# Kernel optimization log

Hardware: AMD Instinct MI355X
Metric: run time of the kernel (lower is better)

## Reference

```python
import jax, jax.numpy as jnp
import numpy as np

B, S, D, H = 2, 2048, 512, 8
HD = D // H  # head_size = 64
EPS = 1e-5


def _layer_norm(x, g, b):
    m = jnp.mean(x, axis=-1, keepdims=True)
    v = jnp.mean(jnp.square(x - m), axis=-1, keepdims=True)
    return (x - m) * jax.lax.rsqrt(v + EPS) * g + b


def setup_inputs() -> dict:
    key = jax.random.key(0)
    ks = jax.random.split(key, 16)
    s_in = 1.0 / np.sqrt(D)
    s_ff = 1.0 / np.sqrt(4 * D)
    return {
        "x": jax.random.normal(ks[0], (B, S, D), jnp.float32),
        # per-head q/k/v projections stacked over heads: [H, D, HD]
        "Wq": jax.random.normal(ks[1], (H, D, HD), jnp.float32) * s_in,
        "bq": jax.random.normal(ks[2], (H, HD), jnp.float32) * s_in,
        "Wk": jax.random.normal(ks[3], (H, D, HD), jnp.float32) * s_in,
        "bk": jax.random.normal(ks[4], (H, HD), jnp.float32) * s_in,
        "Wv": jax.random.normal(ks[5], (H, D, HD), jnp.float32) * s_in,
        "bv": jax.random.normal(ks[6], (H, HD), jnp.float32) * s_in,
        "Wp": jax.random.normal(ks[7], (D, D), jnp.float32) * s_in,
        "bp": jax.random.normal(ks[8], (D,), jnp.float32) * s_in,
        "W1": jax.random.normal(ks[9], (D, 4 * D), jnp.float32) * s_in,
        "b1": jax.random.normal(ks[10], (4 * D,), jnp.float32) * s_in,
        "W2": jax.random.normal(ks[11], (4 * D, D), jnp.float32) * s_ff,
        "b2": jax.random.normal(ks[12], (D,), jnp.float32) * s_ff,
        "g1": jnp.ones((D,), jnp.float32),
        "be1": jnp.zeros((D,), jnp.float32),
        "g2": jnp.ones((D,), jnp.float32),
        "be2": jnp.zeros((D,), jnp.float32),
    }


def reference(x, Wq, bq, Wk, bk, Wv, bv, Wp, bp, W1, b1, W2, b2, g1, be1, g2, be2):
    # --- attention sublayer (pre-norm) ---
    xn = _layer_norm(x, g1, be1)                               # [B,S,D]
    q = jnp.einsum('bsd,hde->bhse', xn, Wq) + bq[None, :, None, :]
    k = jnp.einsum('bsd,hde->bhse', xn, Wk) + bk[None, :, None, :]
    v = jnp.einsum('bsd,hde->bhse', xn, Wv) + bv[None, :, None, :]
    # NOTE: original has NO 1/sqrt(head_size) scaling and NO mask
    scores = jnp.einsum('bhse,bhte->bhst', q, k)               # [B,H,S,S]
    w = jax.nn.softmax(scores, axis=-1)
    o = jnp.einsum('bhst,bhte->bhse', w, v)                    # [B,H,S,HD]
    o = o.transpose(0, 2, 1, 3).reshape(x.shape[0], x.shape[1], D)  # concat heads
    attn_out = o @ Wp + bp
    x = x + attn_out
    # --- MLP sublayer (pre-norm) ---
    xn2 = _layer_norm(x, g2, be2)
    h = jax.nn.relu(xn2 @ W1 + b1)
    x = x + (h @ W2 + b2)
    return x
```

## Files before the change

kernel.cpp:

```cpp
#include <hip/hip_runtime.h>
#include <hip/hip_bf16.h>

typedef unsigned short u16;
typedef unsigned long long u64t;
typedef __attribute__((ext_vector_type(8))) short bhalf8;
typedef __attribute__((ext_vector_type(4))) short bhalf4;
typedef __attribute__((ext_vector_type(4))) float f32x4;

#define MFMA16(a, b, c) __builtin_amdgcn_mfma_f32_16x16x32_bf16((a), (b), (c), 0, 0, 0)

#if __has_builtin(__builtin_amdgcn_mfma_f32_16x16x16bf16_1k)
#define HAVE_K16 1
#define MFMAK16(a, b, c) __builtin_amdgcn_mfma_f32_16x16x16bf16_1k((a), (b), (c), 0, 0, 0)
#elif __has_builtin(__builtin_amdgcn_mfma_f32_16x16x16_bf16)
#define HAVE_K16 1
#define MFMAK16(a, b, c) __builtin_amdgcn_mfma_f32_16x16x16_bf16((a), (b), (c), 0, 0, 0)
#else
#define HAVE_K16 0
#endif

#if __has_builtin(__builtin_amdgcn_perm)
#define HAVE_PERM 1
#else
#define HAVE_PERM 0
#endif

#define BB 2
#define SS 2048
#define DD 512
#define HH 8
#define HD 64
#define NT (BB * SS)
#define LOG2E 1.44269504f

#if __has_builtin(__builtin_amdgcn_exp2f)
#define EXP2(x) __builtin_amdgcn_exp2f(x)
#else
#define EXP2(x) exp2f(x)
#endif

__device__ __forceinline__ u16 f2b(float f) {
    unsigned u = __builtin_bit_cast(unsigned, f);
    unsigned r = (u + 0x7fffu + ((u >> 16) & 1u)) >> 16;
    return (u16)r;
}

__device__ __forceinline__ unsigned pk2bf(float f0, float f1) {
#if HAVE_PERM
    unsigned a0 = __builtin_bit_cast(unsigned, f0) + 0x8000u;
    unsigned a1 = __builtin_bit_cast(unsigned, f1) + 0x8000u;
    return __builtin_amdgcn_perm(a1, a0, 0x07060302u);
#else
    return (unsigned)f2b(f0) | ((unsigned)f2b(f1) << 16);
#endif
}

__device__ __forceinline__ void gl2lds16(const u16* g, u16* l) {
    u16* gn = (u16*)g;
    __builtin_amdgcn_global_load_lds((__attribute__((address_space(1))) void*)gn,
                                     (__attribute__((address_space(3))) void*)l, 16, 0, 0);
}

__global__ __launch_bounds__(256) void k_prep(const float* __restrict__ Wq, const float* __restrict__ Wk,
                                              const float* __restrict__ Wv, const float* __restrict__ Wp,
                                              const float* __restrict__ W1, const float* __restrict__ W2,
                                              const float* __restrict__ bq, const float* __restrict__ bk,
                                              const float* __restrict__ bv,
                                              u16* __restrict__ WqkvT, u16* __restrict__ WpT,
                                              u16* __restrict__ W1T, u16* __restrict__ W2T,
                                              float* __restrict__ biasqkv,
                                              const float* __restrict__ x, const float* __restrict__ g1,
                                              const float* __restrict__ be1, u16* __restrict__ xn) {
    int j = blockIdx.x;
    int t = threadIdx.x;
    if (j >= 3078) {
        int wave = t >> 6, lane = t & 63;
        int row = (j - 3078) * 4 + wave;
        const float* xr = x + (size_t)row * DD;
        int c = lane * 8;
        float4 v0 = *(const float4*)(xr + c);
        float4 v1 = *(const float4*)(xr + c + 4);
        float s  = v0.x + v0.y + v0.z + v0.w + v1.x + v1.y + v1.z + v1.w;
        float sq = v0.x*v0.x + v0.y*v0.y + v0.z*v0.z + v0.w*v0.w
                 + v1.x*v1.x + v1.y*v1.y + v1.z*v1.z + v1.w*v1.w;
#pragma unroll
        for (int m = 1; m < 64; m <<= 1) {
            s  += __shfl_xor(s, m);
            sq += __shfl_xor(sq, m);
        }
        float mean = s * (1.0f / DD);
        float var  = sq * (1.0f / DD) - mean * mean;
        float rstd = rsqrtf(var + 1e-5f);
        float4 g0 = *(const float4*)(g1 + c);
        float4 g4 = *(const float4*)(g1 + c + 4);
        float4 b0 = *(const float4*)(be1 + c);
        float4 b4 = *(const float4*)(be1 + c + 4);
        float xv[8] = {v0.x, v0.y, v0.z, v0.w, v1.x, v1.y, v1.z, v1.w};
        float gv[8] = {g0.x, g0.y, g0.z, g0.w, g4.x, g4.y, g4.z, g4.w};
        float bv2[8] = {b0.x, b0.y, b0.z, b0.w, b4.x, b4.y, b4.z, b4.w};
        union { bhalf8 v; u16 u[8]; } pk;
#pragma unroll
        for (int i = 0; i < 8; i++) pk.u[i] = f2b((xv[i] - mean) * rstd * gv[i] + bv2[i]);
        *(bhalf8*)(xn + (size_t)row * DD + c) = pk.v;
        return;
    }
    int tx = t & 31, ty = t >> 5;
    if (j >= 3072) {
        int i = (j - 3072) * 256 + ty * 32 + tx;
        biasqkv[i] = (i < 512) ? bq[i] : (i < 1024) ? bk[i - 512] : bv[i - 1024];
        return;
    }
    __shared__ float tile[32][33];
    const float* src; u16* dst; int R, C, tr, tc;
    if (j < 768) {
        int m = j >> 8, rem = j & 255, h = rem >> 5, tl = rem & 31;
        tr = tl >> 1; tc = tl & 1;
        src = (m == 0 ? Wq : (m == 1 ? Wk : Wv)) + h * 32768;
        dst = WqkvT + m * 262144 + h * 32768;
        R = 512; C = 64;
    } else if (j < 1024) { int tl = j - 768;  tr = tl >> 4; tc = tl & 15; src = Wp; dst = WpT; R = 512;  C = 512;  }
    else if (j < 2048)   { int tl = j - 1024; tr = tl >> 6; tc = tl & 63; src = W1; dst = W1T; R = 512;  C = 2048; }
    else                 { int tl = j - 2048; tr = tl >> 4; tc = tl & 15; src = W2; dst = W2T; R = 2048; C = 512;  }
    int c = tc * 32 + tx;
#pragma unroll
    for (int i = 0; i < 4; i++)
        tile[ty + i * 8][tx] = src[(size_t)(tr * 32 + ty + i * 8) * C + c];
    __syncthreads();
    int r2 = tr * 32 + tx;
#pragma unroll
    for (int i = 0; i < 4; i++)
        dst[(size_t)(tc * 32 + ty + i * 8) * R + r2] = f2b(tile[tx][ty + i * 8]);
}

__global__ __launch_bounds__(256) void k_layernorm(const float* __restrict__ x,
                                                   const float* __restrict__ g,
                                                   const float* __restrict__ be,
                                                   u16* __restrict__ out) {
    int wave = threadIdx.x >> 6, lane = threadIdx.x & 63;
    int row = blockIdx.x * 4 + wave;
    const float* xr = x + (size_t)row * DD;
    int c = lane * 8;
    float4 v0 = *(const float4*)(xr + c);
    float4 v1 = *(const float4*)(xr + c + 4);
    float s  = v0.x + v0.y + v0.z + v0.w + v1.x + v1.y + v1.z + v1.w;
    float sq = v0.x*v0.x + v0.y*v0.y + v0.z*v0.z + v0.w*v0.w
             + v1.x*v1.x + v1.y*v1.y + v1.z*v1.z + v1.w*v1.w;
#pragma unroll
    for (int m = 1; m < 64; m <<= 1) {
        s  += __shfl_xor(s, m);
        sq += __shfl_xor(sq, m);
    }
    float mean = s * (1.0f / DD);
    float var  = sq * (1.0f / DD) - mean * mean;
    float rstd = rsqrtf(var + 1e-5f);
    float4 g0 = *(const float4*)(g + c);
    float4 g1 = *(const float4*)(g + c + 4);
    float4 b0 = *(const float4*)(be + c);
    float4 b1 = *(const float4*)(be + c + 4);
    float xv[8] = {v0.x, v0.y, v0.z, v0.w, v1.x, v1.y, v1.z, v1.w};
    float gv[8] = {g0.x, g0.y, g0.z, g0.w, g1.x, g1.y, g1.z, g1.w};
    float bv[8] = {b0.x, b0.y, b0.z, b0.w, b1.x, b1.y, b1.z, b1.w};
    union { bhalf8 v; u16 u[8]; } pk;
#pragma unroll
    for (int i = 0; i < 8; i++) pk.u[i] = f2b((xv[i] - mean) * rstd * gv[i] + bv[i]);
    *(bhalf8*)(out + (size_t)row * DD + c) = pk.v;
}

template<int BM, int BN, int WR, int WC, int MI, int NI, int MODE>
__global__ __launch_bounds__(256) void k_gemm(const u16* __restrict__ A, const u16* __restrict__ Bt,
                                              const float* __restrict__ bias,
                                              int lda, int ldb, int kLen, int N,
                                              const float* __restrict__ resid,
                                              float* __restrict__ outF, u16* __restrict__ outB,
                                              u16* __restrict__ qd, u16* __restrict__ kd,
                                              u16* __restrict__ vtd) {
    constexpr int WM = MI * 16;
    constexpr int WN = NI * 16;
    static_assert(WR * WM == BM && WC * WN == BN && WR * WC == 4, "cfg");
    constexpr int ACH = BM / 32;
    constexpr int BCH = BN / 32;
    __shared__ u16 As0[BM * 64];
    __shared__ u16 Bs0[BN * 64];
    __shared__ u16 As1[BM * 64];
    __shared__ u16 Bs1[BN * 64];
    int t = threadIdx.x;
    int wave = t >> 6, lane = t & 63, quad = lane >> 4, l16 = lane & 15;
    int wr, wc;
    if (WC == 1)      { wr = wave; wc = 0; }
    else if (WR == 1) { wr = 0;    wc = wave; }
    else              { wr = wave >> 1; wc = wave & 1; }
    int m0 = blockIdx.y * BM, n0 = blockIdx.x * BN;

    f32x4 acc[MI][NI] = {};

    int srow = lane >> 3;
    int scol = (lane & 7) * 8;
    const u16* Ag = A  + (size_t)(m0 + srow) * lda + scol;
    const u16* Bg = Bt + (size_t)(n0 + srow) * ldb + scol;

    auto stage = [&](u16* Asd, u16* Bsd, int k0) {
#pragma unroll
        for (int c = 0; c < ACH; c++) {
            int ch = wave * ACH + c;
            gl2lds16(Ag + (size_t)(ch * 8) * lda + k0, &Asd[ch * 512]);
        }
#pragma unroll
        for (int c = 0; c < BCH; c++) {
            int ch = wave * BCH + c;
            gl2lds16(Bg + (size_t)(ch * 8) * ldb + k0, &Bsd[ch * 512]);
        }
    };
    auto compute = [&](const u16* Asd, const u16* Bsd) {
#pragma unroll
        for (int h = 0; h < 2; h++) {
            bhalf8 af[MI], bf[NI];
#pragma unroll
            for (int mi = 0; mi < MI; mi++)
                af[mi] = *(const bhalf8*)&Asd[(wr * WM + mi * 16 + l16) * 64 + h * 32 + quad * 8];
#pragma unroll
            for (int ni = 0; ni < NI; ni++)
                bf[ni] = *(const bhalf8*)&Bsd[(wc * WN + ni * 16 + l16) * 64 + h * 32 + quad * 8];
#pragma unroll
            for (int mi = 0; mi < MI; mi++)
#pragma unroll
                for (int ni = 0; ni < NI; ni++)
                    acc[mi][ni] = MFMA16(af[mi], bf[ni], acc[mi][ni]);
        }
    };

    int nt = kLen >> 6;
    stage(As0, Bs0, 0);
    __syncthreads();
    for (int kt = 0; kt < nt; kt += 2) {
        if (kt + 1 < nt) stage(As1, Bs1, (kt + 1) << 6);
        compute(As0, Bs0);
        __syncthreads();
        if (kt + 1 < nt) {
            if (kt + 2 < nt) stage(As0, Bs0, (kt + 2) << 6);
            compute(As1, Bs1);
            __syncthreads();
        }
    }

#pragma unroll
    for (int mi = 0; mi < MI; mi++)
#pragma unroll
        for (int ni = 0; ni < NI; ni++) {
            f32x4 a = acc[mi][ni];
            int gc = n0 + wc * WN + ni * 16 + l16;
            int gr0 = m0 + wr * WM + mi * 16 + quad * 4;
            float bsv = bias[gc];
            if (MODE == 0) {
                int mm = gc >> 9, cc = gc & 511;
                int hh = cc >> 6, e = cc & 63;
                int b = gr0 >> 11, s0 = gr0 & 2047;
                if (mm == 2) {
                    u64t pk = 0;
#pragma unroll
                    for (int r = 0; r < 4; r++) pk |= (u64t)f2b(a[r] + bsv) << (16 * r);
                    *(u64t*)&vtd[((size_t)(b * HH + hh) * HD + e) * SS + s0] = pk;
                } else if (mm == 0) {
#pragma unroll
                    for (int r = 0; r < 4; r++)
                        qd[((size_t)(b * HH + hh) * SS + s0 + r) * HD + e] = f2b((a[r] + bsv) * LOG2E);
                } else {
#pragma unroll
                    for (int r = 0; r < 4; r++)
                        kd[((size_t)(b * HH + hh) * SS + s0 + r) * HD + e] = f2b(a[r] + bsv);
                }
            } else if (MODE == 1) {
#pragma unroll
                for (int r = 0; r < 4; r++) {
                    size_t idx = (size_t)(gr0 + r) * N + gc;
                    outF[idx] = a[r] + bsv + resid[idx];
                }
            } else {
#pragma unroll
                for (int r = 0; r < 4; r++)
                    outB[(size_t)(gr0 + r) * N + gc] = f2b(fmaxf(a[r] + bsv, 0.0f));
            }
        }
}

__global__ __launch_bounds__(512) void k_attention(const u16* __restrict__ q,
                                                   const u16* __restrict__ k,
                                                   const u16* __restrict__ vt,
                                                   float* __restrict__ Opart,
                                                   float* __restrict__ lsum) {
    __shared__ u16 sm[35840];
    u16* Ks0 = sm;
    u16* Vs0 = sm + 9216;
    u16* Ks1 = sm + 17920;
    u16* Vs1 = sm + 27136;
    float* Ored = (float*)sm;
    float* Lred = (float*)sm + 8192;

    int bh = blockIdx.x, qt = blockIdx.y, kspl = blockIdx.z;
    int t = threadIdx.x, wave = t >> 6, lane = t & 63, quad = lane >> 4, l16 = lane & 15;
    int g = wave >> 2, qw = wave & 3;
    const u16* qb = q  + (size_t)bh * SS * HD;
    const u16* kb = k  + (size_t)bh * SS * HD;
    const u16* vb = vt + (size_t)bh * HD * SS;

    bhalf8 qfa0, qfa1, qfb0, qfb1;
    {
        int r0 = qt * 128 + qw * 32 + l16;
        qfa0 = *(const bhalf8*)(qb + (size_t)r0 * HD + quad * 8);
        qfa1 = *(const bhalf8*)(qb + (size_t)r0 * HD + 32 + quad * 8);
        qfb0 = *(const bhalf8*)(qb + (size_t)(r0 + 16) * HD + quad * 8);
        qfb1 = *(const bhalf8*)(qb + (size_t)(r0 + 16) * HD + 32 + quad * 8);
    }

    f32x4 oacc[2][4] = {};
    f32x4 rsa4 = {}, rsb4 = {};

    int kr = t >> 2, kc = (t & 3) * 16;
    int vr = t >> 3, vc = (t & 7) * 16;
    const u16* kp = kb + ((size_t)kspl * 1024 + kr) * HD + kc;
    const u16* vp = vb + (size_t)vr * SS + kspl * 1024 + vc;
    int koff = kr * 72 + kc;
    int voff = vr * 136 + vc;

    bhalf8 kreg[2], vreg[2];
#pragma unroll
    for (int i = 0; i < 2; i++) {
        kreg[i] = *(const bhalf8*)(kp + i * 8);
        vreg[i] = *(const bhalf8*)(vp + i * 8);
    }
#pragma unroll
    for (int i = 0; i < 2; i++) {
        *(bhalf8*)(&Ks0[koff] + i * 8) = kreg[i];
        *(bhalf8*)(&Vs0[voff] + i * 8) = vreg[i];
    }
    __syncthreads();
#pragma unroll
    for (int i = 0; i < 2; i++) {
        kreg[i] = *(const bhalf8*)(kp + (size_t)128 * HD + i * 8);
        vreg[i] = *(const bhalf8*)(vp + 128 + i * 8);
    }

    auto att_step = [&](const u16* Ksb, const u16* Vsb) {
#pragma unroll
        for (int nt2 = 0; nt2 < 4; nt2++) {
            int nt = g * 4 + nt2;
            bhalf8 kf0 = *(const bhalf8*)&Ksb[(nt * 16 + l16) * 72 + quad * 8];
            bhalf8 kf1 = *(const bhalf8*)&Ksb[(nt * 16 + l16) * 72 + 32 + quad * 8];
            f32x4 sa = {}, sb = {};
            __builtin_amdgcn_s_setprio(1);
            sa = MFMA16(kf0, qfa0, sa);
            sa = MFMA16(kf1, qfa1, sa);
            sb = MFMA16(kf0, qfb0, sb);
            sb = MFMA16(kf1, qfb1, sb);
            __builtin_amdgcn_s_setprio(0);
#if HAVE_K16
            float p0[4], p1[4];
#pragma unroll
            for (int r = 0; r < 4; r++) {
                p0[r] = EXP2(sa[r]);
                p1[r] = EXP2(sb[r]);
            }
#pragma unroll
            for (int r = 0; r < 4; r++) { rsa4[r] += p0[r]; rsb4[r] += p1[r]; }
            union { bhalf4 v; unsigned w[2]; } pa, pb;
            pa.w[0] = pk2bf(p0[0], p0[1]);
            pa.w[1] = pk2bf(p0[2], p0[3]);
            pb.w[0] = pk2bf(p1[0], p1[1]);
            pb.w[1] = pk2bf(p1[2], p1[3]);
            __builtin_amdgcn_s_setprio(1);
#pragma unroll
            for (int et = 0; et < 4; et++) {
                bhalf4 vf = *(const bhalf4*)&Vsb[(et * 16 + l16) * 136 + nt * 16 + quad * 4];
                oacc[0][et] = MFMAK16(pa.v, vf, oacc[0][et]);
                oacc[1][et] = MFMAK16(pb.v, vf, oacc[1][et]);
            }
            __builtin_amdgcn_s_setprio(0);
#else
            float p0[4], p1[4];
#pragma unroll
            for (int r = 0; r < 4; r++) {
                p0[r] = EXP2(sa[r]);
                p1[r] = EXP2(sb[r]);
                rsa4[r] += p0[r]; rsb4[r] += p1[r];
            }
            union { bhalf8 v; unsigned w[4]; } pa, pb;
            pa.w[0] = pk2bf(p0[0], p0[1]);
            pa.w[1] = pk2bf(p0[2], p0[3]);
            pa.w[2] = 0; pa.w[3] = 0;
            pb.w[0] = pk2bf(p1[0], p1[1]);
            pb.w[1] = pk2bf(p1[2], p1[3]);
            pb.w[2] = 0; pb.w[3] = 0;
            __builtin_amdgcn_s_setprio(1);
#pragma unroll
            for (int et = 0; et < 4; et++) {
                union { bhalf8 v; bhalf4 h[2]; } vf;
                vf.h[0] = *(const bhalf4*)&Vsb[(et * 16 + l16) * 136 + nt * 16 + quad * 4];
                vf.h[1] = (bhalf4){0, 0, 0, 0};
                oacc[0][et] = MFMA16(pa.v, vf.v, oacc[0][et]);
                oacc[1][et] = MFMA16(pb.v, vf.v, oacc[1][et]);
            }
            __builtin_amdgcn_s_setprio(0);
#endif
        }
    };

    for (int it = 0; it < 8; it += 2) {
#pragma unroll
        for (int i = 0; i < 2; i++) {
            *(bhalf8*)(&Ks1[koff] + i * 8) = kreg[i];
            *(bhalf8*)(&Vs1[voff] + i * 8) = vreg[i];
        }
        if (it + 2 < 8) {
            const u16* kn = kp + (size_t)(it + 2) * 128 * HD;
            const u16* vn = vp + (it + 2) * 128;
#pragma unroll
            for (int i = 0; i < 2; i++) {
                kreg[i] = *(const bhalf8*)(kn + i * 8);
                vreg[i] = *(const bhalf8*)(vn + i * 8);
            }
        }
        att_step(Ks0, Vs0);
        __syncthreads();
        if (it + 2 < 8) {
#pragma unroll
            for (int i = 0; i < 2; i++) {
                *(bhalf8*)(&Ks0[koff] + i * 8) = kreg[i];
                *(bhalf8*)(&Vs0[voff] + i * 8) = vreg[i];
            }
            if (it + 3 < 8) {
                const u16* kn = kp + (size_t)(it + 3) * 128 * HD;
                const u16* vn = vp + (it + 3) * 128;
#pragma unroll
                for (int i = 0; i < 2; i++) {
                    kreg[i] = *(const bhalf8*)(kn + i * 8);
                    vreg[i] = *(const bhalf8*)(vn + i * 8);
                }
            }
        }
        att_step(Ks1, Vs1);
        __syncthreads();
    }

    float rsa = (rsa4[0] + rsa4[1]) + (rsa4[2] + rsa4[3]);
    float rsb = (rsb4[0] + rsb4[1]) + (rsb4[2] + rsb4[3]);
    rsa += __shfl_xor(rsa, 16); rsa += __shfl_xor(rsa, 32);
    rsb += __shfl_xor(rsb, 16); rsb += __shfl_xor(rsb, 32);

    if (g == 1) {
#pragma unroll
        for (int qc = 0; qc < 2; qc++)
#pragma unroll
            for (int et = 0; et < 4; et++)
#pragma unroll
                for (int r = 0; r < 4; r++)
                    Ored[(qw * 32 + qc * 16 + quad * 4 + r) * 64 + et * 16 + l16] = oacc[qc][et][r];
        if (quad == 0) {
            Lred[qw * 32 + l16]      = rsa;
            Lred[qw * 32 + 16 + l16] = rsb;
        }
    }
    __syncthreads();
    if (g == 0) {
#pragma unroll
        for (int qc = 0; qc < 2; qc++) {
            int sbase = qt * 128 + qw * 32 + qc * 16;
            float* Ob = Opart + ((size_t)(kspl * 16 + bh) * SS + sbase) * HD;
#pragma unroll
            for (int et = 0; et < 4; et++)
#pragma unroll
                for (int r = 0; r < 4; r++) {
                    float v = oacc[qc][et][r]
                            + Ored[(qw * 32 + qc * 16 + quad * 4 + r) * 64 + et * 16 + l16];
                    Ob[(quad * 4 + r) * HD + et * 16 + l16] = v;
                }
            if (quad == 0)
                lsum[(size_t)(kspl * 16 + bh) * SS + sbase + l16] =
                    (qc == 0 ? rsa : rsb) + Lred[qw * 32 + qc * 16 + l16];
        }
    }
}

__global__ __launch_bounds__(256) void k_combine(const float* __restrict__ Opart,
                                                 const float* __restrict__ lsum,
                                                 u16* __restrict__ oc) {
    int tid = blockIdx.x * 256 + threadIdx.x;
    int c4 = tid & 15, s = (tid >> 4) & 2047, bh = tid >> 15;
    size_t i0 = ((size_t)bh * SS + s) * HD + c4 * 4;
    float4 p0 = *(const float4*)(Opart + i0);
    float4 p1 = *(const float4*)(Opart + (size_t)16 * SS * HD + i0);
    float l = lsum[(size_t)bh * SS + s] + lsum[(size_t)16 * SS + (size_t)bh * SS + s];
    float inv = 1.0f / l;
    u64t pk = 0;
    pk |= (u64t)f2b((p0.x + p1.x) * inv);
    pk |= (u64t)f2b((p0.y + p1.y) * inv) << 16;
    pk |= (u64t)f2b((p0.z + p1.z) * inv) << 32;
    pk |= (u64t)f2b((p0.w + p1.w) * inv) << 48;
    int b = bh >> 3, h = bh & 7;
    *(u64t*)&oc[((size_t)b * SS + s) * DD + h * HD + c4 * 4] = pk;
}

extern "C" void kernel_launch(void* const* d_in, const int* in_sizes, int n_in,
                              void* d_out, int out_size, void* d_ws, size_t ws_size,
                              hipStream_t stream) {
    const float* x   = (const float*)d_in[0];
    const float* Wq  = (const float*)d_in[1];
    const float* bq  = (const float*)d_in[2];
    const float* Wk  = (const float*)d_in[3];
    const float* bk  = (const float*)d_in[4];
    const float* Wv  = (const float*)d_in[5];
    const float* bv  = (const float*)d_in[6];
    const float* Wp  = (const float*)d_in[7];
    const float* bp  = (const float*)d_in[8];
    const float* W1  = (const float*)d_in[9];
    const float* b1  = (const float*)d_in[10];
    const float* W2  = (const float*)d_in[11];
    const float* b2  = (const float*)d_in[12];
    const float* g1  = (const float*)d_in[13];
    const float* be1 = (const float*)d_in[14];
    const float* g2  = (const float*)d_in[15];
    const float* be2 = (const float*)d_in[16];

    char* ws = (char*)d_ws;
    u16*   WqkvT   = (u16*)(ws + 0);
    u16*   WpT     = (u16*)(ws + 1572864);
    u16*   W1T     = (u16*)(ws + 2097152);
    u16*   W2T     = (u16*)(ws + 4194304);
    float* biasqkv = (float*)(ws + 6291456);
    u16*   xn      = (u16*)(ws + 6297600);
    u16*   qB      = (u16*)(ws + 10491904);
    u16*   kB      = (u16*)(ws + 14686208);
    u16*   vTb     = (u16*)(ws + 18880512);
    u16*   oc      = (u16*)(ws + 23074816);
    float* x1      = (float*)(ws + 27269120);
    u16*   xn2     = (u16*)(ws + 35657728);
    u16*   hbuf    = (u16*)(ws + 39852032);
    float* Opart   = (float*)hbuf;
    float* lsum    = (float*)xn;

    k_prep<<<4102, 256, 0, stream>>>(Wq, Wk, Wv, Wp, W1, W2, bq, bk, bv,
                                     WqkvT, WpT, W1T, W2T, biasqkv,
                                     x, g1, be1, xn);
    k_gemm<128, 128, 2, 2, 4, 4, 0><<<dim3(12, 32), 256, 0, stream>>>(
        xn, WqkvT, biasqkv, 512, 512, 512, 1536, nullptr, nullptr, nullptr, qB, kB, vTb);
    k_attention<<<dim3(16, 16, 2), 512, 0, stream>>>(qB, kB, vTb, Opart, lsum);
    k_combine<<<2048, 256, 0, stream>>>(Opart, lsum, oc);
    k_gemm<64, 64, 2, 2, 2, 2, 1><<<dim3(8, 64), 256, 0, stream>>>(
        oc, WpT, bp, 512, 512, 512, 512, x, x1, nullptr, nullptr, nullptr, nullptr);
    k_layernorm<<<NT / 4, 256, 0, stream>>>(x1, g2, be2, xn2);
    k_gemm<128, 128, 2, 2, 4, 4, 2><<<dim3(16, 32), 256, 0, stream>>>(
        xn2, W1T, b1, 512, 512, 512, 2048, nullptr, nullptr, hbuf, nullptr, nullptr, nullptr);
    k_gemm<64, 64, 2, 2, 2, 2, 1><<<dim3(8, 64), 256, 0, stream>>>(
        hbuf, W2T, b2, 2048, 2048, 2048, 512, x1, (float*)d_out, nullptr, nullptr, nullptr, nullptr);
}
```

Baseline: 199.8 us.

## Drop split-K attention and combine kernel; normalize and write bf16 output in-kernel

Attention no longer splits the key dimension into two halves. Each block instead handles 64 query rows (16 per wave) over all 2048 keys, and the grid changes from 16x16x2 to 16x32. Because each block sees every key, it can normalize by the row sum and write bf16 straight to the concatenated-head output. The separate combine kernel and its fp32 partial-output round trip through memory are removed. The cost is half the MFMA work per K/V tile load: each K/V shared-memory tile now feeds only one 16-row query fragment instead of two, so more K/V traffic is spent per unit of compute.

```diff
diff --git a/kernel.cpp b/kernel.cpp
--- a/kernel.cpp
+++ b/kernel.cpp
@@ -285,39 +285,36 @@
 __global__ __launch_bounds__(512) void k_attention(const u16* __restrict__ q,
                                                    const u16* __restrict__ k,
                                                    const u16* __restrict__ vt,
-                                                   float* __restrict__ Opart,
-                                                   float* __restrict__ lsum) {
+                                                   u16* __restrict__ oc) {
     __shared__ u16 sm[35840];
     u16* Ks0 = sm;
     u16* Vs0 = sm + 9216;
     u16* Ks1 = sm + 17920;
     u16* Vs1 = sm + 27136;
     float* Ored = (float*)sm;
-    float* Lred = (float*)sm + 8192;
-
-    int bh = blockIdx.x, qt = blockIdx.y, kspl = blockIdx.z;
+    float* Lred = (float*)sm + 4096;
+
+    int bh = blockIdx.x, qt = blockIdx.y;
     int t = threadIdx.x, wave = t >> 6, lane = t & 63, quad = lane >> 4, l16 = lane & 15;
     int g = wave >> 2, qw = wave & 3;
     const u16* qb = q  + (size_t)bh * SS * HD;
     const u16* kb = k  + (size_t)bh * SS * HD;
     const u16* vb = vt + (size_t)bh * HD * SS;
 
-    bhalf8 qfa0, qfa1, qfb0, qfb1;
+    bhalf8 qfa0, qfa1;
     {
-        int r0 = qt * 128 + qw * 32 + l16;
+        int r0 = qt * 64 + qw * 16 + l16;
         qfa0 = *(const bhalf8*)(qb + (size_t)r0 * HD + quad * 8);
         qfa1 = *(const bhalf8*)(qb + (size_t)r0 * HD + 32 + quad * 8);
-        qfb0 = *(const bhalf8*)(qb + (size_t)(r0 + 16) * HD + quad * 8);
-        qfb1 = *(const bhalf8*)(qb + (size_t)(r0 + 16) * HD + 32 + quad * 8);
-    }
-
-    f32x4 oacc[2][4] = {};
-    f32x4 rsa4 = {}, rsb4 = {};
+    }
+
+    f32x4 oacc[4] = {};
+    f32x4 rsa4 = {};
 
     int kr = t >> 2, kc = (t & 3) * 16;
     int vr = t >> 3, vc = (t & 7) * 16;
-    const u16* kp = kb + ((size_t)kspl * 1024 + kr) * HD + kc;
-    const u16* vp = vb + (size_t)vr * SS + kspl * 1024 + vc;
+    const u16* kp = kb + (size_t)kr * HD + kc;
+    const u16* vp = vb + (size_t)vr * SS + vc;
     int koff = kr * 72 + kc;
     int voff = vr * 136 + vc;
 
@@ -345,71 +342,58 @@
             int nt = g * 4 + nt2;
             bhalf8 kf0 = *(const bhalf8*)&Ksb[(nt * 16 + l16) * 72 + quad * 8];
             bhalf8 kf1 = *(const bhalf8*)&Ksb[(nt * 16 + l16) * 72 + 32 + quad * 8];
-            f32x4 sa = {}, sb = {};
+            f32x4 sa = {};
             __builtin_amdgcn_s_setprio(1);
             sa = MFMA16(kf0, qfa0, sa);
             sa = MFMA16(kf1, qfa1, sa);
-            sb = MFMA16(kf0, qfb0, sb);
-            sb = MFMA16(kf1, qfb1, sb);
             __builtin_amdgcn_s_setprio(0);
 #if HAVE_K16
-            float p0[4], p1[4];
+            float p0[4];
+#pragma unroll
+            for (int r = 0; r < 4; r++) p0[r] = EXP2(sa[r]);
+#pragma unroll
+            for (int r = 0; r < 4; r++) rsa4[r] += p0[r];
+            union { bhalf4 v; unsigned w[2]; } pa;
+            pa.w[0] = pk2bf(p0[0], p0[1]);
+            pa.w[1] = pk2bf(p0[2], p0[3]);
+            __builtin_amdgcn_s_setprio(1);
+#pragma unroll
+            for (int et = 0; et < 4; et++) {
+                bhalf4 vf = *(const bhalf4*)&Vsb[(et * 16 + l16) * 136 + nt * 16 + quad * 4];
+                oacc[et] = MFMAK16(pa.v, vf, oacc[et]);
+            }
+            __builtin_amdgcn_s_setprio(0);
+#else
+            float p0[4];
 #pragma unroll
             for (int r = 0; r < 4; r++) {
                 p0[r] = EXP2(sa[r]);
-                p1[r] = EXP2(sb[r]);
-            }
-#pragma unroll
-            for (int r = 0; r < 4; r++) { rsa4[r] += p0[r]; rsb4[r] += p1[r]; }
-            union { bhalf4 v; unsigned w[2]; } pa, pb;
-            pa.w[0] = pk2bf(p0[0], p0[1]);
-            pa.w[1] = pk2bf(p0[2], p0[3]);
-            pb.w[0] = pk2bf(p1[0], p1[1]);
-            pb.w[1] = pk2bf(p1[2], p1[3]);
-            __builtin_amdgcn_s_setprio(1);
-#pragma unroll
-            for (int et = 0; et < 4; et++) {
-                bhalf4 vf = *(const bhalf4*)&Vsb[(et * 16 + l16) * 136 + nt * 16 + quad * 4];
-                oacc[0][et] = MFMAK16(pa.v, vf, oacc[0][et]);
-                oacc[1][et] = MFMAK16(pb.v, vf, oacc[1][et]);
-            }
-            __builtin_amdgcn_s_setprio(0);
-#else
-            float p0[4], p1[4];
-#pragma unroll
-            for (int r = 0; r < 4; r++) {
-                p0[r] = EXP2(sa[r]);
-                p1[r] = EXP2(sb[r]);
-                rsa4[r] += p0[r]; rsb4[r] += p1[r];
-            }
-            union { bhalf8 v; unsigned w[4]; } pa, pb;
+                rsa4[r] += p0[r];
+            }
+            union { bhalf8 v; unsigned w[4]; } pa;
             pa.w[0] = pk2bf(p0[0], p0[1]);
             pa.w[1] = pk2bf(p0[2], p0[3]);
             pa.w[2] = 0; pa.w[3] = 0;
-            pb.w[0] = pk2bf(p1[0], p1[1]);
-            pb.w[1] = pk2bf(p1[2], p1[3]);
-            pb.w[2] = 0; pb.w[3] = 0;
             __builtin_amdgcn_s_setprio(1);
 #pragma unroll
             for (int et = 0; et < 4; et++) {
                 union { bhalf8 v; bhalf4 h[2]; } vf;
                 vf.h[0] = *(const bhalf4*)&Vsb[(et * 16 + l16) * 136 + nt * 16 + quad * 4];
                 vf.h[1] = (bhalf4){0, 0, 0, 0};
-                oacc[0][et] = MFMA16(pa.v, vf.v, oacc[0][et]);
-                oacc[1][et] = MFMA16(pb.v, vf.v, oacc[1][et]);
+                oacc[et] = MFMA16(pa.v, vf.v, oacc[et]);
             }
             __builtin_amdgcn_s_setprio(0);
 #endif
         }
     };
 
-    for (int it = 0; it < 8; it += 2) {
+    for (int it = 0; it < 16; it += 2) {
 #pragma unroll
         for (int i = 0; i < 2; i++) {
             *(bhalf8*)(&Ks1[koff] + i * 8) = kreg[i];
             *(bhalf8*)(&Vs1[voff] + i * 8) = vreg[i];
         }
-        if (it + 2 < 8) {
+        if (it + 2 < 16) {
             const u16* kn = kp + (size_t)(it + 2) * 128 * HD;
             const u16* vn = vp + (it + 2) * 128;
 #pragma unroll
@@ -420,13 +404,13 @@
         }
         att_step(Ks0, Vs0);
         __syncthreads();
-        if (it + 2 < 8) {
+        if (it + 2 < 16) {
 #pragma unroll
             for (int i = 0; i < 2; i++) {
                 *(bhalf8*)(&Ks0[koff] + i * 8) = kreg[i];
                 *(bhalf8*)(&Vs0[voff] + i * 8) = vreg[i];
             }
-            if (it + 3 < 8) {
+            if (it + 3 < 16) {
                 const u16* kn = kp + (size_t)(it + 3) * 128 * HD;
                 const u16* vn = vp + (it + 3) * 128;
 #pragma unroll
@@ -441,61 +425,33 @@
     }
 
     float rsa = (rsa4[0] + rsa4[1]) + (rsa4[2] + rsa4[3]);
-    float rsb = (rsb4[0] + rsb4[1]) + (rsb4[2] + rsb4[3]);
     rsa += __shfl_xor(rsa, 16); rsa += __shfl_xor(rsa, 32);
-    rsb += __shfl_xor(rsb, 16); rsb += __shfl_xor(rsb, 32);
 
     if (g == 1) {
 #pragma unroll
-        for (int qc = 0; qc < 2; qc++)
-#pragma unroll
-            for (int et = 0; et < 4; et++)
-#pragma unroll
-                for (int r = 0; r < 4; r++)
-                    Ored[(qw * 32 + qc * 16 + quad * 4 + r) * 64 + et * 16 + l16] = oacc[qc][et][r];
-        if (quad == 0) {
-            Lred[qw * 32 + l16]      = rsa;
-            Lred[qw * 32 + 16 + l16] = rsb;
-        }
+        for (int et = 0; et < 4; et++)
+#pragma unroll
+            for (int r = 0; r < 4; r++)
+                Ored[(qw * 16 + quad * 4 + r) * 64 + et * 16 + l16] = oacc[et][r];
+        if (quad == 0) Lred[qw * 16 + l16] = rsa;
     }
     __syncthreads();
     if (g == 0) {
-#pragma unroll
-        for (int qc = 0; qc < 2; qc++) {
-            int sbase = qt * 128 + qw * 32 + qc * 16;
-            float* Ob = Opart + ((size_t)(kspl * 16 + bh) * SS + sbase) * HD;
-#pragma unroll
-            for (int et = 0; et < 4; et++)
-#pragma unroll
-                for (int r = 0; r < 4; r++) {
-                    float v = oacc[qc][et][r]
-                            + Ored[(qw * 32 + qc * 16 + quad * 4 + r) * 64 + et * 16 + l16];
-                    Ob[(quad * 4 + r) * HD + et * 16 + l16] = v;
-                }
-            if (quad == 0)
-                lsum[(size_t)(kspl * 16 + bh) * SS + sbase + l16] =
-                    (qc == 0 ? rsa : rsb) + Lred[qw * 32 + qc * 16 + l16];
-        }
-    }
-}
-
-__global__ __launch_bounds__(256) void k_combine(const float* __restrict__ Opart,
-                                                 const float* __restrict__ lsum,
-                                                 u16* __restrict__ oc) {
-    int tid = blockIdx.x * 256 + threadIdx.x;
-    int c4 = tid & 15, s = (tid >> 4) & 2047, bh = tid >> 15;
-    size_t i0 = ((size_t)bh * SS + s) * HD + c4 * 4;
-    float4 p0 = *(const float4*)(Opart + i0);
-    float4 p1 = *(const float4*)(Opart + (size_t)16 * SS * HD + i0);
-    float l = lsum[(size_t)bh * SS + s] + lsum[(size_t)16 * SS + (size_t)bh * SS + s];
-    float inv = 1.0f / l;
-    u64t pk = 0;
-    pk |= (u64t)f2b((p0.x + p1.x) * inv);
-    pk |= (u64t)f2b((p0.y + p1.y) * inv) << 16;
-    pk |= (u64t)f2b((p0.z + p1.z) * inv) << 32;
-    pk |= (u64t)f2b((p0.w + p1.w) * inv) << 48;
-    int b = bh >> 3, h = bh & 7;
-    *(u64t*)&oc[((size_t)b * SS + s) * DD + h * HD + c4 * 4] = pk;
+        float inv = 1.0f / (rsa + Lred[qw * 16 + l16]);
+        int b = bh >> 3, h = bh & 7;
+#pragma unroll
+        for (int r = 0; r < 4; r++) {
+            float li = __shfl(inv, quad * 4 + r);
+            int s = qt * 64 + qw * 16 + quad * 4 + r;
+            u16* orow = oc + ((size_t)b * SS + s) * DD + h * HD;
+#pragma unroll
+            for (int et = 0; et < 4; et++) {
+                float v = oacc[et][r]
+                        + Ored[(qw * 16 + quad * 4 + r) * 64 + et * 16 + l16];
+                orow[et * 16 + l16] = f2b(v * li);
+            }
+        }
+    }
 }
 
 extern "C" void kernel_launch(void* const* d_in, const int* in_sizes, int n_in,
@@ -533,16 +489,13 @@
     float* x1      = (float*)(ws + 27269120);
     u16*   xn2     = (u16*)(ws + 35657728);
     u16*   hbuf    = (u16*)(ws + 39852032);
-    float* Opart   = (float*)hbuf;
-    float* lsum    = (float*)xn;
 
     k_prep<<<4102, 256, 0, stream>>>(Wq, Wk, Wv, Wp, W1, W2, bq, bk, bv,
                                      WqkvT, WpT, W1T, W2T, biasqkv,
                                      x, g1, be1, xn);
     k_gemm<128, 128, 2, 2, 4, 4, 0><<<dim3(12, 32), 256, 0, stream>>>(
         xn, WqkvT, biasqkv, 512, 512, 512, 1536, nullptr, nullptr, nullptr, qB, kB, vTb);
-    k_attention<<<dim3(16, 16, 2), 512, 0, stream>>>(qB, kB, vTb, Opart, lsum);
-    k_combine<<<2048, 256, 0, stream>>>(Opart, lsum, oc);
+    k_attention<<<dim3(16, 32), 512, 0, stream>>>(qB, kB, vTb, oc);
     k_gemm<64, 64, 2, 2, 2, 2, 1><<<dim3(8, 64), 256, 0, stream>>>(
         oc, WpT, bp, 512, 512, 512, 512, x, x1, nullptr, nullptr, nullptr, nullptr);
     k_layernorm<<<NT / 4, 256, 0, stream>>>(x1, g2, be2, xn2);
```

New measurement: 193.9 us. 1.03x faster.
